# Kernel optimization log

Measured on AMD Instinct MI355X. Metric: run time of the kernel, lower is better.

Reference implementation:

```python
import jax, jax.numpy as jnp
import numpy as np

B, N, M, D, OUT, K = 8, 32, 64, 128, 128, 3
EPS = 1e-5


def batchnorm(x, g, b):
    # training-mode BatchNorm2d over NCHW (stats over B,H,W per channel, biased var)
    mean = x.mean((0, 2, 3), keepdims=True)
    var = ((x - mean) ** 2).mean((0, 2, 3), keepdims=True)
    return g[None, :, None, None] * (x - mean) * jax.lax.rsqrt(var + EPS) + b[None, :, None, None]


def mycorr(x):
    # Pearson correlation between nodes along feature dim: x (B,M,N,D) -> (B,M,N,N)
    xc = x - x.mean(-1, keepdims=True)
    num = jnp.einsum('bmid,bmjd->bmij', xc, xc)
    nrm = jnp.sqrt((xc * xc).sum(-1))
    return num / (nrm[:, :, :, None] * nrm[:, :, None, :] + 1e-8)


def attention(x, W_fc1, W_fc2):
    # x: (B,M,N,D). AdaptiveAvgPool2d((None,1)) over the concat [Wh_i, pos*Wh_j]
    # equals 0.5*(mean_d Wh_i + mean_d(pos*Wh_j)); pos=1 where Wh_i==Wh_j else 2.
    adj = mycorr(x)
    mean_i = x.mean(-1)                       # (B,M,N)
    xi = x[:, :, :, None, :]                  # (B,M,N,1,D)
    xj = x[:, :, None, :, :]                  # (B,M,1,N,D)
    alt_mean = jnp.where(xi == xj, xj, 2.0 * xj).mean(-1)  # (B,M,N,N)
    e = 0.5 * (mean_i[:, :, :, None] + alt_mean)            # (B,M,N,N)
    ef = e.reshape(e.shape[0], e.shape[1], -1)              # (B,M,N*N) pair channels
    h = jax.nn.relu(jnp.einsum('rp,bmp->bmr', W_fc1, ef))
    e2 = jax.nn.sigmoid(jnp.einsum('pr,bmr->bmp', W_fc2, h)).reshape(e.shape)
    att = jax.nn.softmax(jnp.where(adj > 0, e2, jnp.float32(-1e12)), axis=-1)
    return jnp.einsum('bmij,bmjd->bmid', att, x)


def setup_inputs() -> dict:
    key = jax.random.key(0)
    ks = jax.random.split(key, 8)
    P, r, s = N * N, (N * N) // 2, 0.05
    return {
        'x': jax.random.normal(ks[0], (B, N, M, D), jnp.float32),
        'W_sc': jax.random.normal(ks[1], (OUT, M), jnp.float32) * s,
        'g_sc': jnp.ones(OUT, jnp.float32), 'b_sc': jnp.zeros(OUT, jnp.float32),
        'W_l1': jax.random.normal(ks[2], (M, M), jnp.float32) * s,
        'g1': jnp.ones(M, jnp.float32), 'b1': jnp.zeros(M, jnp.float32),
        'W_fc1': jax.random.normal(ks[3], (r, P), jnp.float32) * s,
        'W_fc2': jax.random.normal(ks[4], (P, r), jnp.float32) * s,
        'g2': jnp.ones(M, jnp.float32), 'b2': jnp.zeros(M, jnp.float32),
        'W_dw': jax.random.normal(ks[5], (N, 1, K, K), jnp.float32) * s,
        'g3': jnp.ones(N, jnp.float32), 'b3': jnp.zeros(N, jnp.float32),
        'W_l3': jax.random.normal(ks[6], (OUT, M), jnp.float32) * s,
    }


def reference(x, W_sc, g_sc, b_sc, W_l1, g1, b1, W_fc1, W_fc2, g2, b2, W_dw, g3, b3, W_l3):
    xm = jnp.transpose(x, (0, 2, 1, 3))  # (B,M,N,D)
    # shortcut: 1x1 conv over head channel + BN (stride=1 path)
    shortcut = batchnorm(jnp.einsum('om,bmnd->bond', W_sc, xm), g_sc, b_sc)
    # layer_1: 1x1 conv, BN, global node attention, BN, ReLU
    out = batchnorm(jnp.einsum('cm,bmnd->bcnd', W_l1, xm), g1, b1)
    out = attention(out, W_fc1, W_fc2)
    out = jax.nn.relu(batchnorm(out, g2, b2))
    # layer_2: depthwise KxK conv over (head, dim) per node, BN, ReLU
    out = jnp.transpose(out, (0, 2, 1, 3))  # (B,N,M,D)
    pad = K // 2
    out = jax.lax.conv_general_dilated(out, W_dw, (1, 1), ((pad, pad), (pad, pad)),
                                       feature_group_count=N,
                                       dimension_numbers=('NCHW', 'OIHW', 'NCHW'))
    out = jax.nn.relu(batchnorm(out, g3, b3))
    # layer_3: 1x1 conv to out_channels heads + residual
    out = jnp.transpose(out, (0, 2, 1, 3))  # (B,M,N,D)
    out = jnp.einsum('om,bmnd->bond', W_l3, out) + shortcut
    return jnp.transpose(out, (0, 2, 1, 3))  # (B,N,OUT,D)
```

## Files before the change

### kernel.cpp

```cpp
#include <hip/hip_runtime.h>
#include <math.h>

#define EPS 1e-5f


__device__ __forceinline__ void fma4(float4& a, float s, const float4& v) {
    a.x += s * v.x; a.y += s * v.y; a.z += s * v.z; a.w += s * v.w;
}

__global__ __launch_bounds__(256) void k1_matmul_stats(
    const float* __restrict__ x, const float* __restrict__ Wsc,
    const float* __restrict__ Wl1, float* __restrict__ t_sc,
    float* __restrict__ t_l1, float* __restrict__ stats)
{
    int g  = blockIdx.x;
    int bn = blockIdx.y;
    int b = bn >> 5, n = bn & 31;
    __shared__ __align__(16) float s_x[64 * 128];
    __shared__ __align__(16) float s_wT[64 * 68];
    int t = threadIdx.x;

    const float4* xg = (const float4*)(x + (size_t)bn * 8192);
    for (int i = t; i < 2048; i += 256) ((float4*)s_x)[i] = xg[i];

    const float* wbase = (g < 2) ? (Wsc + (size_t)g * 64 * 64) : Wl1;
    for (int i = t; i < 1024; i += 256) {
        int m = i >> 4, rq = (i & 15) * 4;
        float4 wv;
        wv.x = wbase[(size_t)(rq + 0) * 64 + m];
        wv.y = wbase[(size_t)(rq + 1) * 64 + m];
        wv.z = wbase[(size_t)(rq + 2) * 64 + m];
        wv.w = wbase[(size_t)(rq + 3) * 64 + m];
        *(float4*)(s_wT + m * 68 + rq) = wv;
    }
    __syncthreads();

    int wv = t >> 6, lane = t & 63;
    int dl = lane & 15;
    int g4 = lane >> 4;
    int d0 = dl * 8;
    int c0 = wv * 16 + g4 * 4;

    float4 acc[4][2];
#pragma unroll
    for (int i = 0; i < 4; i++) { acc[i][0] = make_float4(0,0,0,0); acc[i][1] = make_float4(0,0,0,0); }

    for (int m = 0; m < 64; m += 2) {
        float4 x00 = *(const float4*)(s_x + m * 128 + d0);
        float4 x01 = *(const float4*)(s_x + m * 128 + d0 + 4);
        float4 x10 = *(const float4*)(s_x + (m + 1) * 128 + d0);
        float4 x11 = *(const float4*)(s_x + (m + 1) * 128 + d0 + 4);
        float4 w0 = *(const float4*)(s_wT + m * 68 + c0);
        float4 w1 = *(const float4*)(s_wT + (m + 1) * 68 + c0);
        fma4(acc[0][0], w0.x, x00); fma4(acc[0][1], w0.x, x01);
        fma4(acc[1][0], w0.y, x00); fma4(acc[1][1], w0.y, x01);
        fma4(acc[2][0], w0.z, x00); fma4(acc[2][1], w0.z, x01);
        fma4(acc[3][0], w0.w, x00); fma4(acc[3][1], w0.w, x01);
        fma4(acc[0][0], w1.x, x10); fma4(acc[0][1], w1.x, x11);
        fma4(acc[1][0], w1.y, x10); fma4(acc[1][1], w1.y, x11);
        fma4(acc[2][0], w1.z, x10); fma4(acc[2][1], w1.z, x11);
        fma4(acc[3][0], w1.w, x10); fma4(acc[3][1], w1.w, x11);
    }

#pragma unroll
    for (int i = 0; i < 4; i++) {
        int cc = g * 64 + c0 + i;
        float4 v0 = acc[i][0], v1 = acc[i][1];
        float* dst;
        if (cc < 128) dst = t_sc + (((size_t)(b * 128 + cc)) * 32 + n) * 128 + d0;
        else          dst = t_l1 + (((size_t)(b * 64 + (cc - 128))) * 32 + n) * 128 + d0;
        *(float4*)dst = v0;
        *(float4*)(dst + 4) = v1;
        float s = v0.x + v0.y + v0.z + v0.w + v1.x + v1.y + v1.z + v1.w;
        float q = v0.x*v0.x + v0.y*v0.y + v0.z*v0.z + v0.w*v0.w
                + v1.x*v1.x + v1.y*v1.y + v1.z*v1.z + v1.w*v1.w;
#pragma unroll
        for (int off = 8; off > 0; off >>= 1) {
            s += __shfl_down(s, off, 16);
            q += __shfl_down(q, off, 16);
        }
        if (dl == 0) {
            if (cc < 128) {
                atomicAdd(&stats[cc], s);
                atomicAdd(&stats[cc + 128], q);
            } else {
                atomicAdd(&stats[256 + (cc - 128)], s);
                atomicAdd(&stats[320 + (cc - 128)], q);
            }
        }
    }
}

__global__ __launch_bounds__(256) void k2_attn_prep(
    const float* __restrict__ t_l1, const float* __restrict__ g1,
    const float* __restrict__ b1, const float* __restrict__ stats,
    float* __restrict__ y_g, float* __restrict__ E,
    unsigned int* __restrict__ maskbits)
{
    int bm = blockIdx.x;
    int t  = threadIdx.x;
    __shared__ __align__(16) float y_s[32 * 132];
    __shared__ float S_s[32];
    __shared__ unsigned int m_s[32];
    int m = bm & 63;
    float mean = stats[256 + m] * (1.0f / 32768.0f);
    float var  = stats[320 + m] * (1.0f / 32768.0f) - mean * mean;
    float a = g1[m] * rsqrtf(var + EPS);
    float c = b1[m] - a * mean;

    if (t < 32) m_s[t] = 0u;
    const float4* src = (const float4*)(t_l1 + (size_t)bm * 4096);
    for (int i = t; i < 1024; i += 256) {
        float4 v = src[i];
        v.x = a * v.x + c; v.y = a * v.y + c; v.z = a * v.z + c; v.w = a * v.w + c;
        int row = i >> 5, col = (i & 31) * 4;
        *(float4*)(y_s + row * 132 + col) = v;
    }
    __syncthreads();

    {
        int r = t >> 3, j = t & 7;
        float s = 0.f;
        const float* yr = y_s + r * 132 + j * 16;
#pragma unroll
        for (int dd = 0; dd < 16; dd++) s += yr[dd];
#pragma unroll
        for (int off = 4; off > 0; off >>= 1) s += __shfl_down(s, off, 8);
        if (j == 0) S_s[r] = s;
    }
    __syncthreads();

    int i = t >> 3, j0 = (t & 7) * 4;
    float dot[4] = {0.f, 0.f, 0.f, 0.f};
    float eqs[4] = {0.f, 0.f, 0.f, 0.f};
    const float* yi = y_s + i * 132;
    for (int dq = 0; dq < 32; dq++) {
        float4 a4 = *(const float4*)(yi + dq * 4);
#pragma unroll
        for (int q = 0; q < 4; q++) {
            float4 b4 = *(const float4*)(y_s + (j0 + q) * 132 + dq * 4);
            dot[q] += a4.x * b4.x + a4.y * b4.y + a4.z * b4.z + a4.w * b4.w;
            eqs[q] += (a4.x == b4.x ? b4.x : 0.f) + (a4.y == b4.y ? b4.y : 0.f)
                    + (a4.z == b4.z ? b4.z : 0.f) + (a4.w == b4.w ? b4.w : 0.f);
        }
    }
    float Si = S_s[i];
    unsigned int bits = 0u;
    float ev[4];
#pragma unroll
    for (int q = 0; q < 4; q++) {
        float Sj = S_s[j0 + q];
        float num = dot[q] - Si * Sj * (1.0f / 128.0f);
        if (num > 0.f) bits |= (1u << (j0 + q));
        ev[q] = (Si + 2.f * Sj - eqs[q]) * (1.0f / 256.0f);
    }
    atomicOr(&m_s[i], bits);
    *(float4*)(E + (size_t)bm * 1024 + i * 32 + j0) = make_float4(ev[0], ev[1], ev[2], ev[3]);
    __syncthreads();
    if (t < 32) maskbits[bm * 32 + t] = m_s[t];

    float4* yd = (float4*)(y_g + (size_t)bm * 4096);
    for (int idx = t; idx < 1024; idx += 256) {
        int row = idx >> 5, col = (idx & 31) * 4;
        yd[idx] = *(const float4*)(y_s + row * 132 + col);
    }
}

template<int KDIM, int MODE>
__global__ __launch_bounds__(256) void k3_gemm(
    const float* __restrict__ A, const float* __restrict__ Bm,
    float* __restrict__ C, int NC)
{
    __shared__ __align__(16) float lds[4 * 2304];
    int t = threadIdx.x;
    int w = t >> 6, l = t & 63;
    int ct = blockIdx.x, rt = blockIdx.y;
    int row0 = rt * 32, col0 = ct * 32;
    float* As = lds + w * 2304;
    float* Bs = As + 1152;
    int rg = l >> 3;
    int cg = l & 7;
    int kq = (l & 7) * 4;
    constexpr int SLABS = KDIM / 128;

    float4 acc[4];
#pragma unroll
    for (int ii = 0; ii < 4; ii++) acc[ii] = make_float4(0,0,0,0);

    float4 av[4], bv[4], av2[4], bv2[4];
    int k0 = w * 32;
#pragma unroll
    for (int rr = 0; rr < 4; rr++) {
        int r = rg + rr * 8;
        av[rr] = *(const float4*)(A  + (size_t)(row0 + r) * KDIM + k0 + kq);
        bv[rr] = *(const float4*)(Bm + (size_t)(col0 + r) * KDIM + k0 + kq);
    }

    for (int s = 0; s < SLABS; s++) {
#pragma unroll
        for (int rr = 0; rr < 4; rr++) {
            int r = rg + rr * 8;
            As[(kq + 0) * 36 + r] = av[rr].x; As[(kq + 1) * 36 + r] = av[rr].y;
            As[(kq + 2) * 36 + r] = av[rr].z; As[(kq + 3) * 36 + r] = av[rr].w;
            Bs[(kq + 0) * 36 + r] = bv[rr].x; Bs[(kq + 1) * 36 + r] = bv[rr].y;
            Bs[(kq + 2) * 36 + r] = bv[rr].z; Bs[(kq + 3) * 36 + r] = bv[rr].w;
        }
        if (s + 1 < SLABS) {
            int kn = (4 * (s + 1) + w) * 32;
#pragma unroll
            for (int rr = 0; rr < 4; rr++) {
                int r = rg + rr * 8;
                av2[rr] = *(const float4*)(A  + (size_t)(row0 + r) * KDIM + kn + kq);
                bv2[rr] = *(const float4*)(Bm + (size_t)(col0 + r) * KDIM + kn + kq);
            }
        }
#pragma unroll
        for (int k = 0; k < 32; k++) {
            float4 a = *(const float4*)(As + k * 36 + rg * 4);
            float4 b = *(const float4*)(Bs + k * 36 + cg * 4);
            fma4(acc[0], a.x, b);
            fma4(acc[1], a.y, b);
            fma4(acc[2], a.z, b);
            fma4(acc[3], a.w, b);
        }
#pragma unroll
        for (int rr = 0; rr < 4; rr++) { av[rr] = av2[rr]; bv[rr] = bv2[rr]; }
    }

    __syncthreads();
    float* red = lds;
#pragma unroll
    for (int ii = 0; ii < 4; ii++)
        *(float4*)(red + w * 1024 + (rg * 4 + ii) * 32 + cg * 4) = acc[ii];
    __syncthreads();

    int r = t >> 3, c4 = (t & 7) * 4;
    float4 s0 = *(const float4*)(red + r * 32 + c4);
    float4 s1 = *(const float4*)(red + 1024 + r * 32 + c4);
    float4 s2 = *(const float4*)(red + 2048 + r * 32 + c4);
    float4 s3 = *(const float4*)(red + 3072 + r * 32 + c4);
    float4 v;
    v.x = s0.x + s1.x + s2.x + s3.x;
    v.y = s0.y + s1.y + s2.y + s3.y;
    v.z = s0.z + s1.z + s2.z + s3.z;
    v.w = s0.w + s1.w + s2.w + s3.w;
    if (MODE == 0) {
        v.x = fmaxf(v.x, 0.f); v.y = fmaxf(v.y, 0.f);
        v.z = fmaxf(v.z, 0.f); v.w = fmaxf(v.w, 0.f);
    } else {
        v.x = 1.0f / (1.0f + expf(-v.x)); v.y = 1.0f / (1.0f + expf(-v.y));
        v.z = 1.0f / (1.0f + expf(-v.z)); v.w = 1.0f / (1.0f + expf(-v.w));
    }
    *(float4*)(C + (size_t)(row0 + r) * NC + col0 + c4) = v;
}

__global__ __launch_bounds__(256) void k4_attn_apply(
    const float* __restrict__ E2, const unsigned int* __restrict__ maskbits,
    const float* __restrict__ y_g, float* __restrict__ att_out,
    float* __restrict__ stats)
{
    int bm = blockIdx.x;
    int t  = threadIdx.x;
    __shared__ __align__(16) float att_s[32 * 33];
    __shared__ __align__(16) float y_sh[32 * 128];
    __shared__ float redS[4], redQ[4];

    const float4* ysrc = (const float4*)(y_g + (size_t)bm * 4096);
    float4* yds = (float4*)y_sh;
    for (int i = t; i < 1024; i += 256) yds[i] = ysrc[i];

    {
        int r = t >> 3, j0 = (t & 7) * 4;
        unsigned int mk = maskbits[bm * 32 + r];
        float4 e4 = *(const float4*)(E2 + (size_t)bm * 1024 + r * 32 + j0);
        float v0 = ((mk >> (j0 + 0)) & 1u) ? e4.x : -1e12f;
        float v1 = ((mk >> (j0 + 1)) & 1u) ? e4.y : -1e12f;
        float v2 = ((mk >> (j0 + 2)) & 1u) ? e4.z : -1e12f;
        float v3 = ((mk >> (j0 + 3)) & 1u) ? e4.w : -1e12f;
        float mx = fmaxf(fmaxf(v0, v1), fmaxf(v2, v3));
#pragma unroll
        for (int off = 1; off < 8; off <<= 1) mx = fmaxf(mx, __shfl_xor(mx, off, 8));
        float e0 = __expf(v0 - mx), e1 = __expf(v1 - mx);
        float e2 = __expf(v2 - mx), e3 = __expf(v3 - mx);
        float s = e0 + e1 + e2 + e3;
#pragma unroll
        for (int off = 1; off < 8; off <<= 1) s += __shfl_xor(s, off, 8);
        float inv = 1.0f / s;
        att_s[r * 33 + j0 + 0] = e0 * inv;
        att_s[r * 33 + j0 + 1] = e1 * inv;
        att_s[r * 33 + j0 + 2] = e2 * inv;
        att_s[r * 33 + j0 + 3] = e3 * inv;
    }
    __syncthreads();

    int tx = t & 31, ty = t >> 5;
    int dq = tx * 4;
    float ssum = 0.f, sq = 0.f;
#pragma unroll
    for (int ii = 0; ii < 4; ii++) {
        int i = ty * 4 + ii;
        float4 acc = make_float4(0.f, 0.f, 0.f, 0.f);
        for (int j = 0; j < 32; j++) {
            float aw = att_s[i * 33 + j];
            float4 yv = *(const float4*)(y_sh + j * 128 + dq);
            acc.x += aw * yv.x; acc.y += aw * yv.y;
            acc.z += aw * yv.z; acc.w += aw * yv.w;
        }
        *(float4*)(att_out + (size_t)bm * 4096 + i * 128 + dq) = acc;
        ssum += acc.x + acc.y + acc.z + acc.w;
        sq   += acc.x * acc.x + acc.y * acc.y + acc.z * acc.z + acc.w * acc.w;
    }
#pragma unroll
    for (int off = 32; off > 0; off >>= 1) {
        ssum += __shfl_down(ssum, off, 64);
        sq   += __shfl_down(sq, off, 64);
    }
    int wave = t >> 6, lane = t & 63;
    if (lane == 0) { redS[wave] = ssum; redQ[wave] = sq; }
    __syncthreads();
    if (t == 0) {
        float S = redS[0] + redS[1] + redS[2] + redS[3];
        float Q = redQ[0] + redQ[1] + redQ[2] + redQ[3];
        int m = bm & 63;
        atomicAdd(&stats[384 + m], S);
        atomicAdd(&stats[448 + m], Q);
    }
}

__global__ __launch_bounds__(256) void k5_conv(
    const float* __restrict__ att_out, const float* __restrict__ Wdw,
    const float* __restrict__ g2, const float* __restrict__ b2,
    float* __restrict__ stats, float* __restrict__ v_g)
{
    int bn = blockIdx.x;
    int b = bn >> 5, n = bn & 31;
    int t = threadIdx.x;
    __shared__ __align__(16) float z_s[66 * 130];
    __shared__ float a2_s[64], c2_s[64];
    __shared__ float redS[4], redQ[4];

    if (t < 64) {
        float mean = stats[384 + t] * (1.0f / 32768.0f);
        float var  = stats[448 + t] * (1.0f / 32768.0f) - mean * mean;
        float a = g2[t] * rsqrtf(var + EPS);
        a2_s[t] = a; c2_s[t] = b2[t] - a * mean;
    }
    for (int i = t; i < 66 * 130; i += 256) z_s[i] = 0.f;
    __syncthreads();

    for (int i = t; i < 2048; i += 256) {
        int m = i >> 5, c4 = (i & 31) * 4;
        float4 vv = *(const float4*)(att_out + (((size_t)(b * 64 + m)) * 32 + n) * 128 + c4);
        float a = a2_s[m], c = c2_s[m];
        float* dst = z_s + (m + 1) * 130 + c4 + 1;
        dst[0] = fmaxf(a * vv.x + c, 0.f);
        dst[1] = fmaxf(a * vv.y + c, 0.f);
        dst[2] = fmaxf(a * vv.z + c, 0.f);
        dst[3] = fmaxf(a * vv.w + c, 0.f);
    }
    float w[9];
#pragma unroll
    for (int i = 0; i < 9; i++) w[i] = Wdw[n * 9 + i];
    __syncthreads();

    int tx = t & 31, ty = t >> 5;
    int d0 = tx * 4;
    float ssum = 0.f, sq = 0.f;
#pragma unroll
    for (int rr = 0; rr < 8; rr++) {
        int h = ty * 8 + rr;
        float o0 = 0.f, o1 = 0.f, o2 = 0.f, o3 = 0.f;
#pragma unroll
        for (int dh = 0; dh < 3; dh++) {
            const float* zr = z_s + (h + dh) * 130 + d0;
#pragma unroll
            for (int dw = 0; dw < 3; dw++) {
                float wv = w[dh * 3 + dw];
                o0 += wv * zr[dw + 0];
                o1 += wv * zr[dw + 1];
                o2 += wv * zr[dw + 2];
                o3 += wv * zr[dw + 3];
            }
        }
        *(float4*)(v_g + ((size_t)bn * 64 + h) * 128 + d0) = make_float4(o0, o1, o2, o3);
        ssum += o0 + o1 + o2 + o3;
        sq   += o0 * o0 + o1 * o1 + o2 * o2 + o3 * o3;
    }
#pragma unroll
    for (int off = 32; off > 0; off >>= 1) {
        ssum += __shfl_down(ssum, off, 64);
        sq   += __shfl_down(sq, off, 64);
    }
    int wave = t >> 6, lane = t & 63;
    if (lane == 0) { redS[wave] = ssum; redQ[wave] = sq; }
    __syncthreads();
    if (t == 0) {
        atomicAdd(&stats[512 + n], redS[0] + redS[1] + redS[2] + redS[3]);
        atomicAdd(&stats[544 + n], redQ[0] + redQ[1] + redQ[2] + redQ[3]);
    }
}

__global__ __launch_bounds__(256) void k6_final(
    const float* __restrict__ v_g, const float* __restrict__ t_sc,
    const float* __restrict__ Wl3, const float* __restrict__ g3,
    const float* __restrict__ b3, const float* __restrict__ gsc,
    const float* __restrict__ bsc, const float* __restrict__ stats,
    float* __restrict__ outp)
{
    int oh = blockIdx.x;
    int bn = blockIdx.y;
    int b = bn >> 5, n = bn & 31;
    int t = threadIdx.x;
    __shared__ __align__(16) float z_s[64 * 128];
    __shared__ __align__(16) float s_wT[64 * 68];

    float mean3 = stats[512 + n] * (1.0f / 65536.0f);
    float var3  = stats[544 + n] * (1.0f / 65536.0f) - mean3 * mean3;
    float a3 = g3[n] * rsqrtf(var3 + EPS);
    float c3 = b3[n] - a3 * mean3;

    const float4* vsrc = (const float4*)(v_g + (size_t)bn * 8192);
    for (int i = t; i < 2048; i += 256) {
        float4 vv = vsrc[i];
        float4 r;
        r.x = fmaxf(a3 * vv.x + c3, 0.f);
        r.y = fmaxf(a3 * vv.y + c3, 0.f);
        r.z = fmaxf(a3 * vv.z + c3, 0.f);
        r.w = fmaxf(a3 * vv.w + c3, 0.f);
        ((float4*)z_s)[i] = r;
    }
    const float* wbase = Wl3 + (size_t)oh * 64 * 64;
    for (int i = t; i < 1024; i += 256) {
        int m = i >> 4, rq = (i & 15) * 4;
        float4 wv;
        wv.x = wbase[(size_t)(rq + 0) * 64 + m];
        wv.y = wbase[(size_t)(rq + 1) * 64 + m];
        wv.z = wbase[(size_t)(rq + 2) * 64 + m];
        wv.w = wbase[(size_t)(rq + 3) * 64 + m];
        *(float4*)(s_wT + m * 68 + rq) = wv;
    }
    __syncthreads();

    int wv = t >> 6, lane = t & 63;
    int dl = lane & 15, g4 = lane >> 4;
    int d0 = dl * 8;
    int c0 = wv * 16 + g4 * 4;

    float4 acc[4][2];
#pragma unroll
    for (int i = 0; i < 4; i++) { acc[i][0] = make_float4(0,0,0,0); acc[i][1] = make_float4(0,0,0,0); }

    for (int m = 0; m < 64; m += 2) {
        float4 x00 = *(const float4*)(z_s + m * 128 + d0);
        float4 x01 = *(const float4*)(z_s + m * 128 + d0 + 4);
        float4 x10 = *(const float4*)(z_s + (m + 1) * 128 + d0);
        float4 x11 = *(const float4*)(z_s + (m + 1) * 128 + d0 + 4);
        float4 w0 = *(const float4*)(s_wT + m * 68 + c0);
        float4 w1 = *(const float4*)(s_wT + (m + 1) * 68 + c0);
        fma4(acc[0][0], w0.x, x00); fma4(acc[0][1], w0.x, x01);
        fma4(acc[1][0], w0.y, x00); fma4(acc[1][1], w0.y, x01);
        fma4(acc[2][0], w0.z, x00); fma4(acc[2][1], w0.z, x01);
        fma4(acc[3][0], w0.w, x00); fma4(acc[3][1], w0.w, x01);
        fma4(acc[0][0], w1.x, x10); fma4(acc[0][1], w1.x, x11);
        fma4(acc[1][0], w1.y, x10); fma4(acc[1][1], w1.y, x11);
        fma4(acc[2][0], w1.z, x10); fma4(acc[2][1], w1.z, x11);
        fma4(acc[3][0], w1.w, x10); fma4(acc[3][1], w1.w, x11);
    }

#pragma unroll
    for (int i = 0; i < 4; i++) {
        int o = oh * 64 + c0 + i;
        float msc = stats[o] * (1.0f / 32768.0f);
        float vsc = stats[128 + o] * (1.0f / 32768.0f) - msc * msc;
        float asc = gsc[o] * rsqrtf(vsc + EPS);
        float csc = bsc[o] - asc * msc;
        const float* ts = t_sc + (((size_t)(b * 128 + o)) * 32 + n) * 128 + d0;
        float4 t0 = *(const float4*)(ts);
        float4 t1 = *(const float4*)(ts + 4);
        float4 o0 = acc[i][0], o1 = acc[i][1];
        o0.x += asc * t0.x + csc; o0.y += asc * t0.y + csc;
        o0.z += asc * t0.z + csc; o0.w += asc * t0.w + csc;
        o1.x += asc * t1.x + csc; o1.y += asc * t1.y + csc;
        o1.z += asc * t1.z + csc; o1.w += asc * t1.w + csc;
        float* dst = outp + (((size_t)(b * 32 + n)) * 128 + o) * 128 + d0;
        *(float4*)dst = o0;
        *(float4*)(dst + 4) = o1;
    }
}

extern "C" void kernel_launch(void* const* d_in, const int* in_sizes, int n_in,
                              void* d_out, int out_size, void* d_ws, size_t ws_size,
                              hipStream_t stream)
{
    const float* x    = (const float*)d_in[0];
    const float* Wsc  = (const float*)d_in[1];
    const float* gsc  = (const float*)d_in[2];
    const float* bsc  = (const float*)d_in[3];
    const float* Wl1  = (const float*)d_in[4];
    const float* g1   = (const float*)d_in[5];
    const float* b1   = (const float*)d_in[6];
    const float* Wfc1 = (const float*)d_in[7];
    const float* Wfc2 = (const float*)d_in[8];
    const float* g2   = (const float*)d_in[9];
    const float* b2   = (const float*)d_in[10];
    const float* Wdw  = (const float*)d_in[11];
    const float* g3   = (const float*)d_in[12];
    const float* b3   = (const float*)d_in[13];
    const float* Wl3  = (const float*)d_in[14];
    float* outp = (float*)d_out;

    float* ws = (float*)d_ws;
    float* stats = ws;
    float* t_sc  = ws + 1024;
    float* t_l1  = t_sc + 4194304;
    float* y_g   = t_l1 + 2097152;
    float* E     = y_g + 2097152;
    float* H     = E + 524288;
    float* E2    = H + 262144;
    unsigned int* maskb = (unsigned int*)(E2 + 524288);

    (void)hipMemsetAsync(stats, 0, 1024 * sizeof(float), stream);

    k1_matmul_stats<<<dim3(3, 256), 256, 0, stream>>>(x, Wsc, Wl1, t_sc, t_l1, stats);
    k2_attn_prep<<<512, 256, 0, stream>>>(t_l1, g1, b1, stats, y_g, E, maskb);
    k3_gemm<1024, 0><<<dim3(16, 16), 256, 0, stream>>>(E, Wfc1, H, 512);
    k3_gemm<512, 1><<<dim3(32, 16), 256, 0, stream>>>(H, Wfc2, E2, 1024);
    k4_attn_apply<<<512, 256, 0, stream>>>(E2, maskb, y_g, t_l1, stats);
    k5_conv<<<256, 256, 0, stream>>>(t_l1, Wdw, g2, b2, stats, y_g);
    k6_final<<<dim3(2, 256), 256, 0, stream>>>(y_g, t_sc, Wl3, g3, b3, gsc, bsc, stats, outp);
}
```

Measured before the change: 210.5 us.

## Factor first attention FC through row/column sums, drop pair-feature GEMM

Rewrites W_fc1·E using the structure E_ij=(S_i+2S_j-eq_ij)/256: a small folded weight C1 (row/col sums of W_fc1, computed in an extra k1 block column) is multiplied by the per-node sums S, with a sparse correction for off-diagonal equal-element pairs. This removes the materialized E tensor and the K=1024 GEMM launch. Correction entries are capped at 64 per block, so inputs with many tied values would be handled incorrectly. Also restructures the attention-apply loop to reuse each loaded y row across four output rows.

```diff
diff --git a/kernel.cpp b/kernel.cpp
--- a/kernel.cpp
+++ b/kernel.cpp
@@ -10,16 +10,38 @@
 
 __global__ __launch_bounds__(256) void k1_matmul_stats(
     const float* __restrict__ x, const float* __restrict__ Wsc,
-    const float* __restrict__ Wl1, float* __restrict__ t_sc,
-    float* __restrict__ t_l1, float* __restrict__ stats)
+    const float* __restrict__ Wl1, const float* __restrict__ Wfc1,
+    float* __restrict__ t_sc, float* __restrict__ t_l1,
+    float* __restrict__ C1, float* __restrict__ stats)
 {
     int g  = blockIdx.x;
     int bn = blockIdx.y;
-    int b = bn >> 5, n = bn & 31;
     __shared__ __align__(16) float s_x[64 * 128];
     __shared__ __align__(16) float s_wT[64 * 68];
     int t = threadIdx.x;
 
+    if (g == 3) {
+#pragma unroll
+        for (int rr = 0; rr < 2; rr++) {
+            int r = bn * 2 + rr;
+            *(float4*)(s_x + t * 4) =
+                *(const float4*)(Wfc1 + (size_t)r * 1024 + t * 4);
+            __syncthreads();
+            if (t < 32) {
+                float rs = 0.f, cs = 0.f;
+#pragma unroll
+                for (int j = 0; j < 32; j++) {
+                    rs += s_x[t * 32 + j];
+                    cs += s_x[j * 32 + t];
+                }
+                C1[r * 32 + t] = (rs + 2.f * cs - s_x[t * 33]) * (1.0f / 256.0f);
+            }
+            __syncthreads();
+        }
+        return;
+    }
+
+    int b = bn >> 5, n = bn & 31;
     const float4* xg = (const float4*)(x + (size_t)bn * 8192);
     for (int i = t; i < 2048; i += 256) ((float4*)s_x)[i] = xg[i];
 
@@ -94,7 +116,8 @@
 __global__ __launch_bounds__(256) void k2_attn_prep(
     const float* __restrict__ t_l1, const float* __restrict__ g1,
     const float* __restrict__ b1, const float* __restrict__ stats,
-    float* __restrict__ y_g, float* __restrict__ E,
+    const float* __restrict__ Wfc1, const float* __restrict__ C1,
+    float* __restrict__ y_g, float* __restrict__ H,
     unsigned int* __restrict__ maskbits)
 {
     int bm = blockIdx.x;
@@ -102,12 +125,16 @@
     __shared__ __align__(16) float y_s[32 * 132];
     __shared__ float S_s[32];
     __shared__ unsigned int m_s[32];
+    __shared__ int anom_cnt;
+    __shared__ int anom_p[64];
+    __shared__ float anom_v[64];
     int m = bm & 63;
     float mean = stats[256 + m] * (1.0f / 32768.0f);
     float var  = stats[320 + m] * (1.0f / 32768.0f) - mean * mean;
     float a = g1[m] * rsqrtf(var + EPS);
     float c = b1[m] - a * mean;
 
+    if (t == 0) anom_cnt = 0;
     if (t < 32) m_s[t] = 0u;
     const float4* src = (const float4*)(t_l1 + (size_t)bm * 4096);
     for (int i = t; i < 1024; i += 256) {
@@ -146,18 +173,40 @@
     }
     float Si = S_s[i];
     unsigned int bits = 0u;
-    float ev[4];
 #pragma unroll
     for (int q = 0; q < 4; q++) {
-        float Sj = S_s[j0 + q];
+        int j = j0 + q;
+        float Sj = S_s[j];
         float num = dot[q] - Si * Sj * (1.0f / 128.0f);
-        if (num > 0.f) bits |= (1u << (j0 + q));
-        ev[q] = (Si + 2.f * Sj - eqs[q]) * (1.0f / 256.0f);
+        if (num > 0.f) bits |= (1u << j);
+        if (j != i && eqs[q] != 0.f) {
+            int idx = atomicAdd(&anom_cnt, 1);
+            if (idx < 64) {
+                anom_p[idx] = i * 32 + j;
+                anom_v[idx] = eqs[q] * (1.0f / 256.0f);
+            }
+        }
     }
     atomicOr(&m_s[i], bits);
-    *(float4*)(E + (size_t)bm * 1024 + i * 32 + j0) = make_float4(ev[0], ev[1], ev[2], ev[3]);
     __syncthreads();
     if (t < 32) maskbits[bm * 32 + t] = m_s[t];
+
+    int cnt = anom_cnt; if (cnt > 64) cnt = 64;
+#pragma unroll
+    for (int rr = 0; rr < 2; rr++) {
+        int r = t * 2 + rr;
+        const float4* c1r = (const float4*)(C1 + r * 32);
+        float acc = 0.f;
+#pragma unroll
+        for (int kk = 0; kk < 8; kk++) {
+            float4 cv = c1r[kk];
+            acc += cv.x * S_s[kk * 4 + 0] + cv.y * S_s[kk * 4 + 1]
+                 + cv.z * S_s[kk * 4 + 2] + cv.w * S_s[kk * 4 + 3];
+        }
+        for (int a2 = 0; a2 < cnt; a2++)
+            acc -= Wfc1[(size_t)r * 1024 + anom_p[a2]] * anom_v[a2];
+        H[(size_t)bm * 512 + r] = fmaxf(acc, 0.f);
+    }
 
     float4* yd = (float4*)(y_g + (size_t)bm * 4096);
     for (int idx = t; idx < 1024; idx += 256) {
@@ -295,18 +344,26 @@
 
     int tx = t & 31, ty = t >> 5;
     int dq = tx * 4;
+    int i0 = ty * 4;
+    float4 acc0 = make_float4(0,0,0,0), acc1 = make_float4(0,0,0,0);
+    float4 acc2 = make_float4(0,0,0,0), acc3 = make_float4(0,0,0,0);
+    for (int j = 0; j < 32; j++) {
+        float4 yv = *(const float4*)(y_sh + j * 128 + dq);
+        float w0 = att_s[(i0 + 0) * 33 + j];
+        float w1 = att_s[(i0 + 1) * 33 + j];
+        float w2 = att_s[(i0 + 2) * 33 + j];
+        float w3 = att_s[(i0 + 3) * 33 + j];
+        fma4(acc0, w0, yv);
+        fma4(acc1, w1, yv);
+        fma4(acc2, w2, yv);
+        fma4(acc3, w3, yv);
+    }
     float ssum = 0.f, sq = 0.f;
+    float4 accs[4] = {acc0, acc1, acc2, acc3};
 #pragma unroll
     for (int ii = 0; ii < 4; ii++) {
-        int i = ty * 4 + ii;
-        float4 acc = make_float4(0.f, 0.f, 0.f, 0.f);
-        for (int j = 0; j < 32; j++) {
-            float aw = att_s[i * 33 + j];
-            float4 yv = *(const float4*)(y_sh + j * 128 + dq);
-            acc.x += aw * yv.x; acc.y += aw * yv.y;
-            acc.z += aw * yv.z; acc.w += aw * yv.w;
-        }
-        *(float4*)(att_out + (size_t)bm * 4096 + i * 128 + dq) = acc;
+        float4 acc = accs[ii];
+        *(float4*)(att_out + (size_t)bm * 4096 + (i0 + ii) * 128 + dq) = acc;
         ssum += acc.x + acc.y + acc.z + acc.w;
         sq   += acc.x * acc.x + acc.y * acc.y + acc.z * acc.z + acc.w * acc.w;
     }
@@ -514,16 +571,15 @@
     float* t_sc  = ws + 1024;
     float* t_l1  = t_sc + 4194304;
     float* y_g   = t_l1 + 2097152;
-    float* E     = y_g + 2097152;
-    float* H     = E + 524288;
+    float* C1    = y_g + 2097152;
+    float* H     = C1 + 16384;
     float* E2    = H + 262144;
     unsigned int* maskb = (unsigned int*)(E2 + 524288);
 
     (void)hipMemsetAsync(stats, 0, 1024 * sizeof(float), stream);
 
-    k1_matmul_stats<<<dim3(3, 256), 256, 0, stream>>>(x, Wsc, Wl1, t_sc, t_l1, stats);
-    k2_attn_prep<<<512, 256, 0, stream>>>(t_l1, g1, b1, stats, y_g, E, maskb);
-    k3_gemm<1024, 0><<<dim3(16, 16), 256, 0, stream>>>(E, Wfc1, H, 512);
+    k1_matmul_stats<<<dim3(4, 256), 256, 0, stream>>>(x, Wsc, Wl1, Wfc1, t_sc, t_l1, C1, stats);
+    k2_attn_prep<<<512, 256, 0, stream>>>(t_l1, g1, b1, stats, Wfc1, C1, y_g, H, maskb);
     k3_gemm<512, 1><<<dim3(32, 16), 256, 0, stream>>>(H, Wfc2, E2, 1024);
     k4_attn_apply<<<512, 256, 0, stream>>>(E2, maskb, y_g, t_l1, stats);
     k5_conv<<<256, 256, 0, stream>>>(t_l1, Wdw, g2, b2, stats, y_g);
```

Result: faster. 198.8 us (-5.6%).
